# Performance work log

Hardware: AMD Instinct MI355X
Metric: run time of the kernel (lower is better)

Reference implementation:

```python
import jax, jax.numpy as jnp
import numpy as np

N_NODES = 50000
N_EDGES = 800000
D_IN, D_HID, N_CLS = 128, 64, 40


def setup_inputs() -> dict:
    key = jax.random.key(0)
    ks = jax.random.split(key, 12)
    x = jax.random.normal(ks[0], (N_NODES, D_IN), dtype=jnp.float32)
    edge_index = jax.random.randint(ks[1], (2, N_EDGES), 0, N_NODES, dtype=jnp.int64)
    s = 0.05
    return {
        "x": x,
        "edge_index": edge_index,
        # layer 1 params
        "W1": jax.random.normal(ks[2], (D_IN, D_HID), dtype=jnp.float32) * s,
        "aW1": jax.random.normal(ks[3], (2 * D_HID, 1), dtype=jnp.float32) * s,
        "ab1": jnp.zeros((1,), dtype=jnp.float32),
        "b1": jnp.zeros((D_HID,), dtype=jnp.float32),
        # layer 2 params
        "W2": jax.random.normal(ks[4], (D_HID, D_HID), dtype=jnp.float32) * s,
        "aW2": jax.random.normal(ks[5], (2 * D_HID, 1), dtype=jnp.float32) * s,
        "ab2": jnp.zeros((1,), dtype=jnp.float32),
        "b2": jnp.zeros((D_HID,), dtype=jnp.float32),
        # output head
        "Wo": jax.random.normal(ks[6], (D_HID, N_CLS), dtype=jnp.float32) * s,
        "bo": jnp.zeros((N_CLS,), dtype=jnp.float32),
    }


def _gat_layer(x, src, dst, W, aW, ab, bias, n_nodes):
    h = x @ W                                    # [N, out]
    s = h[src]                                   # [E, out] gather source feats
    t = h[dst]                                   # [E, out] gather target feats
    # per-edge attention score, leaky_relu(negative_slope=0.2)
    sim = jax.nn.leaky_relu(jnp.concatenate([s, t], axis=-1) @ aW + ab,
                            negative_slope=0.2)[:, 0]        # [E]
    # scatter-softmax over incoming edges of each dst node
    m = jax.ops.segment_max(sim, dst, num_segments=n_nodes)   # [N]
    e = jnp.exp(sim - m[dst])
    z = jax.ops.segment_sum(e, dst, num_segments=n_nodes)     # [N]
    a = e / z[dst]                                             # [E]
    msg = a[:, None] * s                                       # [E, out]
    out = jax.ops.segment_max(msg, dst, num_segments=n_nodes)  # scatter-max aggr
    return out + bias


def reference(x, edge_index, W1, aW1, ab1, b1, W2, aW2, ab2, b2, Wo, bo):
    n = x.shape[0]
    loop = jnp.arange(n, dtype=edge_index.dtype)
    src = jnp.concatenate([edge_index[0], loop])  # add self loops
    dst = jnp.concatenate([edge_index[1], loop])
    h = jax.nn.relu(_gat_layer(x, src, dst, W1, aW1, ab1, b1, n))
    h = jax.nn.relu(_gat_layer(h, src, dst, W2, aW2, ab2, b2, n))
    logits = h @ Wo + bo
    return jax.nn.log_softmax(logits, axis=-1)
```

## Files before the change

kernel.cpp:

```cpp
#include <hip/hip_runtime.h>
#include <hip/hip_fp16.h>
#include <math.h>

#define N_NODES 50000
#define N_EDGES 800000
#define E_TOT   (N_EDGES + N_NODES)
#define D_HID   64
#define N_CLS   40
#define SCAN_B  256
#define N_CHUNKS ((N_NODES + SCAN_B - 1) / SCAN_B)
#define NB      391
#define EPB     4096

struct __align__(8) H4 { __half2 a, b; };

__device__ __forceinline__ unsigned pk_max_f16(unsigned a, unsigned b) {
    unsigned r;
    asm("v_pk_max_f16 %0, %1, %2" : "=v"(r) : "v"(a), "v"(b));
    return r;
}
__device__ __forceinline__ unsigned pk_mul_f16(unsigned a, unsigned b) {
    unsigned r;
    asm("v_pk_mul_f16 %0, %1, %2" : "=v"(r) : "v"(a), "v"(b));
    return r;
}
__device__ __forceinline__ unsigned pkmax_xor(unsigned v, int o) {
    unsigned t = __shfl_xor((int)v, o, 64);
    return pk_max_f16(v, t);
}

__global__ void k_convert(const void* ei, int2* __restrict__ pairs,
                          int* __restrict__ deg) {
    __shared__ int s_is32;
    if (threadIdx.x == 0) s_is32 = 0;
    __syncthreads();
    const int* p32 = (const int*)ei;
    if (p32[2 * threadIdx.x + 1] != 0) atomicOr(&s_is32, 1);
    __syncthreads();
    int e = blockIdx.x * 256 + threadIdx.x;
    if (e >= N_EDGES) return;
    int s, d;
    if (s_is32) {
        s = p32[e]; d = p32[N_EDGES + e];
    } else {
        const long long* p64 = (const long long*)ei;
        s = (int)p64[e]; d = (int)p64[N_EDGES + e];
    }
    pairs[e] = make_int2(s, d);
    atomicAdd(&deg[d], 1);
}

__device__ __forceinline__ int block_scan_incl(int v, int* wsum) {
    int lane = threadIdx.x & 63, w = threadIdx.x >> 6;
    int s = v;
#pragma unroll
    for (int d = 1; d < 64; d <<= 1) {
        int t = __shfl_up(s, d, 64);
        if (lane >= d) s += t;
    }
    if (lane == 63) wsum[w] = s;
    __syncthreads();
    int add = 0;
    for (int ww = 0; ww < (threadIdx.x >> 6); ++ww) add += wsum[ww];
    return s + add;
}

__global__ void k_scan1(const int* __restrict__ deg, int* __restrict__ rowptr,
                        int* __restrict__ partials) {
    __shared__ int wsum[4];
    int i = blockIdx.x * SCAN_B + threadIdx.x;
    int v = (i < N_NODES) ? deg[i] + 1 : 0;
    int s = block_scan_incl(v, wsum);
    if (i < N_NODES) rowptr[i] = s - v;
    if (threadIdx.x == SCAN_B - 1) partials[blockIdx.x] = s;
}

__global__ void k_scan2(int* partials) {
    __shared__ int wsum[4];
    int i = threadIdx.x;
    int v = (i < N_CHUNKS) ? partials[i] : 0;
    int s = block_scan_incl(v, wsum);
    if (i < N_CHUNKS) partials[i] = s - v;
}

__global__ void k_scan3(const int* __restrict__ partials, int* __restrict__ rowptr) {
    int i = blockIdx.x * SCAN_B + threadIdx.x;
    if (i < N_NODES) rowptr[i] += partials[blockIdx.x];
    if (blockIdx.x == 0 && threadIdx.x == 0) rowptr[N_NODES] = E_TOT;
}

__global__ void k_bucket_init(const int* __restrict__ rowptr, int* __restrict__ bcursor) {
    int b = threadIdx.x;
    if (b < NB) bcursor[b] = rowptr[b << 7] - (b << 7);
}

__global__ __launch_bounds__(256) void k_bucket_scatter(
        const int2* __restrict__ pairs_in, int* __restrict__ bcursor,
        int2* __restrict__ pairs_bkt) {
    __shared__ int counts[512];
    __shared__ int gbase[512];
    int t = threadIdx.x;
    counts[t] = 0; counts[t + 256] = 0;
    __syncthreads();
    int base = blockIdx.x * EPB;
    int nEdge = min(EPB, N_EDGES - base);
    int2 pr0, pr1, pr2, pr3, pr4, pr5, pr6, pr7, pr8, pr9, prA, prB, prC, prD, prE, prF;
    int rk[16], bk[16];
#define LOADI(i, pv) { int idx = t + (i) * 256;                        \
        if (idx < nEdge) { pv = pairs_in[base + idx];                   \
            bk[i] = pv.y >> 7; rk[i] = atomicAdd(&counts[bk[i]], 1); } }
    LOADI(0, pr0) LOADI(1, pr1) LOADI(2, pr2) LOADI(3, pr3)
    LOADI(4, pr4) LOADI(5, pr5) LOADI(6, pr6) LOADI(7, pr7)
    LOADI(8, pr8) LOADI(9, pr9) LOADI(10, prA) LOADI(11, prB)
    LOADI(12, prC) LOADI(13, prD) LOADI(14, prE) LOADI(15, prF)
#undef LOADI
    __syncthreads();
    if (counts[t])       gbase[t]       = atomicAdd(&bcursor[t], counts[t]);
    if (counts[t + 256]) gbase[t + 256] = atomicAdd(&bcursor[t + 256], counts[t + 256]);
    __syncthreads();
#define STOREI(i, pv) { int idx = t + (i) * 256;                        \
        if (idx < nEdge) pairs_bkt[gbase[bk[i]] + rk[i]] = pv; }
    STOREI(0, pr0) STOREI(1, pr1) STOREI(2, pr2) STOREI(3, pr3)
    STOREI(4, pr4) STOREI(5, pr5) STOREI(6, pr6) STOREI(7, pr7)
    STOREI(8, pr8) STOREI(9, pr9) STOREI(10, prA) STOREI(11, prB)
    STOREI(12, prC) STOREI(13, prD) STOREI(14, prE) STOREI(15, prF)
#undef STOREI
}

__global__ __launch_bounds__(256) void k_bucket_place(
        const int2* __restrict__ pairs_bkt, const int* __restrict__ rowptr,
        int* __restrict__ src_sorted) {
    __shared__ int cur[128];
    int b = blockIdx.x, t = threadIdx.x;
    int d0 = b << 7;
    int dEnd = min(d0 + 128, N_NODES);
    if (t < 128) {
        int d = d0 + t;
        if (d < dEnd) {
            int r = rowptr[d];
            src_sorted[r] = d;
            cur[t] = r + 1;
        }
    }
    __syncthreads();
    int pbase = rowptr[d0] - d0;
    int pend  = rowptr[dEnd] - dEnd;
    for (int idx = pbase + t; idx < pend; idx += 256) {
        int2 p = pairs_bkt[idx];
        int pos = atomicAdd(&cur[p.y - d0], 1);
        src_sorted[pos] = p.x;
    }
}

template<int K>
__global__ __launch_bounds__(256, 4) void k_gemm_alpha(
        const float* __restrict__ x, const float* __restrict__ W,
        const float* __restrict__ aW,
        H4* __restrict__ WhH,
        float* __restrict__ alpha_s, float* __restrict__ alpha_t) {
    __shared__ float Wc[32][68];
    __shared__ float xT[32][68];
    int tid = threadIdx.x;
    int tx2 = tid & 15, ty2 = tid >> 4;
    int rowBase = blockIdx.x * 64;

    float acc[4][4];
#pragma unroll
    for (int r = 0; r < 4; ++r)
#pragma unroll
        for (int c = 0; c < 4; ++c) acc[r][c] = 0.f;

    int rr = tid >> 2;
    int kk = (tid & 3) * 8;
    int srcRow = min(rowBase + rr, N_NODES - 1);
    const float* xrow = x + (size_t)srcRow * K;
    int wrow = tid >> 3;
    int wcol = (tid & 7) * 8;

    for (int kb = 0; kb < K; kb += 32) {
        __syncthreads();
        float4 a0 = *(const float4*)(xrow + kb + kk);
        float4 a1 = *(const float4*)(xrow + kb + kk + 4);
        float4 w0 = *(const float4*)(W + (size_t)(kb + wrow) * 64 + wcol);
        float4 w1 = *(const float4*)(W + (size_t)(kb + wrow) * 64 + wcol + 4);
        xT[kk + 0][rr] = a0.x; xT[kk + 1][rr] = a0.y;
        xT[kk + 2][rr] = a0.z; xT[kk + 3][rr] = a0.w;
        xT[kk + 4][rr] = a1.x; xT[kk + 5][rr] = a1.y;
        xT[kk + 6][rr] = a1.z; xT[kk + 7][rr] = a1.w;
        *(float4*)&Wc[wrow][wcol] = w0;
        *(float4*)&Wc[wrow][wcol + 4] = w1;
        __syncthreads();
#pragma unroll 8
        for (int k2 = 0; k2 < 32; ++k2) {
            float4 xa = *(const float4*)&xT[k2][ty2 * 4];
            float4 wb = *(const float4*)&Wc[k2][tx2 * 4];
            acc[0][0] = fmaf(xa.x, wb.x, acc[0][0]);
            acc[0][1] = fmaf(xa.x, wb.y, acc[0][1]);
            acc[0][2] = fmaf(xa.x, wb.z, acc[0][2]);
            acc[0][3] = fmaf(xa.x, wb.w, acc[0][3]);
            acc[1][0] = fmaf(xa.y, wb.x, acc[1][0]);
            acc[1][1] = fmaf(xa.y, wb.y, acc[1][1]);
            acc[1][2] = fmaf(xa.y, wb.z, acc[1][2]);
            acc[1][3] = fmaf(xa.y, wb.w, acc[1][3]);
            acc[2][0] = fmaf(xa.z, wb.x, acc[2][0]);
            acc[2][1] = fmaf(xa.z, wb.y, acc[2][1]);
            acc[2][2] = fmaf(xa.z, wb.z, acc[2][2]);
            acc[2][3] = fmaf(xa.z, wb.w, acc[2][3]);
            acc[3][0] = fmaf(xa.w, wb.x, acc[3][0]);
            acc[3][1] = fmaf(xa.w, wb.y, acc[3][1]);
            acc[3][2] = fmaf(xa.w, wb.z, acc[3][2]);
            acc[3][3] = fmaf(xa.w, wb.w, acc[3][3]);
        }
    }

    float4 as4 = *(const float4*)(aW + tx2 * 4);
    float4 at4 = *(const float4*)(aW + 64 + tx2 * 4);
#pragma unroll
    for (int r = 0; r < 4; ++r) {
        int row = rowBase + ty2 * 4 + r;
        if (row >= N_NODES) continue;
        H4 hv;
        hv.a = __floats2half2_rn(acc[r][0], acc[r][1]);
        hv.b = __floats2half2_rn(acc[r][2], acc[r][3]);
        WhH[(size_t)row * 16 + tx2] = hv;
        float ps = acc[r][0] * as4.x + acc[r][1] * as4.y + acc[r][2] * as4.z + acc[r][3] * as4.w;
        float pt = acc[r][0] * at4.x + acc[r][1] * at4.y + acc[r][2] * at4.z + acc[r][3] * at4.w;
#pragma unroll
        for (int o = 1; o < 16; o <<= 1) {
            ps += __shfl_xor(ps, o, 64);
            pt += __shfl_xor(pt, o, 64);
        }
        if (tx2 == 0) { alpha_s[row] = ps; alpha_t[row] = pt; }
    }
}

__device__ void slow_node(int rs, int re, const int* __restrict__ src_sorted,
                          const float* __restrict__ alpha_s, float at,
                          const H4* __restrict__ WhH, int lane, int fl2,
                          float& z, unsigned vm[4]) {
    float m = -INFINITY;
    for (int base = rs; base < re; base += 64) {
        int idx = base + lane;
        float sim = -INFINITY;
        if (idx < re) {
            int sv = src_sorted[idx];
            float t = alpha_s[sv] + at;
            sim = t > 0.f ? t : 0.2f * t;
        }
#pragma unroll
        for (int o = 32; o; o >>= 1) sim = fmaxf(sim, __shfl_xor(sim, o, 64));
        m = fmaxf(m, sim);
    }
    z = 0.f;
    float vsc = -INFINITY;
    for (int base = rs; base < re; base += 64) {
        int idx = base + lane;
        int cnt = min(64, re - base);
        int svv = 0;
        float ev = 0.f;
        if (idx < re) {
            svv = src_sorted[idx];
            float t = alpha_s[svv] + at;
            t = t > 0.f ? t : 0.2f * t;
            ev = __expf(t - m);
        }
        float sz = ev;
#pragma unroll
        for (int o = 32; o; o >>= 1) sz += __shfl_xor(sz, o, 64);
        z += sz;
        for (int j = 0; j < cnt; ++j) {
            int sj = __shfl(svv, j, 64);
            float ej = __shfl(ev, j, 64);
            float v = __half2float(((const __half*)WhH)[(size_t)sj * 64 + lane]);
            vsc = fmaxf(vsc, ej * v);
        }
    }
#pragma unroll
    for (int q = 0; q < 4; ++q) {
        float a0 = __shfl(vsc, fl2 * 8 + 2 * q, 64);
        float a1 = __shfl(vsc, fl2 * 8 + 2 * q + 1, 64);
        __half2 p = __floats2half2_rn(a0, a1);
        vm[q] = *(unsigned*)&p;
    }
}

template<int HEAD>
__global__ void k_node_aggr(const int* __restrict__ rowptr, const int* __restrict__ src_sorted,
                            const float* __restrict__ alpha_s, const float* __restrict__ alpha_t,
                            const float* __restrict__ ab, const H4* __restrict__ WhH,
                            const float* __restrict__ bias,
                            const float* __restrict__ Wo, const float* __restrict__ bo,
                            float* __restrict__ outp) {
    __shared__ float sWo[HEAD ? 64 * N_CLS : 1];
    __shared__ float sh[HEAD ? 8 * 64 : 1];
    int lane = threadIdx.x, w = threadIdx.y;
    if (HEAD) {
        int tid = w * 64 + lane;
        for (int i = tid; i < 64 * N_CLS; i += 256) sWo[i] = Wo[i];
    }
    int dA = blockIdx.x * 8 + w * 2;
    int dB = dA + 1;
    int rsA = rowptr[dA], reA = rowptr[dA + 1];
    int rsB = rowptr[dB], reB = rowptr[dB + 1];
    int degA = reA - rsA, degB = reB - rsB;
    float abv = ab[0];
    float atA = alpha_t[dA] + abv;
    float atB = alpha_t[dB] + abv;
    int g2 = lane >> 3, fl2 = lane & 7;
    const char* whb = (const char*)WhH;

    float zA, zB;
    unsigned vmA[4], vmB[4];

    if (degA <= 64 && degB <= 64) {
        int svA = src_sorted[rsA + min(lane, degA - 1)];
        int svB = src_sorted[rsB + min(lane, degB - 1)];
        float tA = alpha_s[svA] + atA; tA = tA > 0.f ? tA : 0.2f * tA;
        float tB = alpha_s[svB] + atB; tB = tB > 0.f ? tB : 0.2f * tB;
        float evA = __expf(tA);
        float evB = __expf(tB);
        float zzA = (lane < degA) ? evA : 0.f;
        float zzB = (lane < degB) ? evB : 0.f;
#pragma unroll
        for (int o = 32; o; o >>= 1) {
            zzA += __shfl_xor(zzA, o, 64);
            zzB += __shfl_xor(zzB, o, 64);
        }
        zA = zzA; zB = zzB;
        int ofsA = svA * 128, ofsB = svB * 128;

        const unsigned NEGINF2 = 0xFC00FC00u;
        unsigned vA0 = NEGINF2, vA1 = NEGINF2, vA2 = NEGINF2, vA3 = NEGINF2;
        unsigned vB0 = NEGINF2, vB1 = NEGINF2, vB2 = NEGINF2, vB3 = NEGINF2;
#define ROUND(ev, ofs, deg, v0, v1, v2, v3, r) { \
        int j = (r) * 8 + g2; j = j < (deg) ? j : (deg) - 1;              \
        float ej = __shfl((ev), j, 64);                                   \
        int ro = __shfl((ofs), j, 64);                                    \
        uint4 hv = *(const uint4*)(whb + ro + fl2 * 16);                  \
        __half2 ejh = __float2half2_rn(ej);                               \
        unsigned ej2 = *(unsigned*)&ejh;                                  \
        v0 = pk_max_f16(v0, pk_mul_f16(ej2, hv.x));                       \
        v1 = pk_max_f16(v1, pk_mul_f16(ej2, hv.y));                       \
        v2 = pk_max_f16(v2, pk_mul_f16(ej2, hv.z));                       \
        v3 = pk_max_f16(v3, pk_mul_f16(ej2, hv.w)); }
#define RA(r) ROUND(evA, ofsA, degA, vA0, vA1, vA2, vA3, r)
#define RB(r) ROUND(evB, ofsB, degB, vB0, vB1, vB2, vB3, r)

        RA(0) RB(0) RA(1) RB(1)
        if (degA > 16) { RA(2) RA(3) }
        if (degB > 16) { RB(2) RB(3) }
        if (degA > 32) { RA(4) RA(5) RA(6) RA(7) }
        if (degB > 32) { RB(4) RB(5) RB(6) RB(7) }
#undef RA
#undef RB
#undef ROUND
#pragma unroll
        for (int o = 8; o <= 32; o <<= 1) {
            vA0 = pkmax_xor(vA0, o); vA1 = pkmax_xor(vA1, o);
            vA2 = pkmax_xor(vA2, o); vA3 = pkmax_xor(vA3, o);
            vB0 = pkmax_xor(vB0, o); vB1 = pkmax_xor(vB1, o);
            vB2 = pkmax_xor(vB2, o); vB3 = pkmax_xor(vB3, o);
        }
        vmA[0] = vA0; vmA[1] = vA1; vmA[2] = vA2; vmA[3] = vA3;
        vmB[0] = vB0; vmB[1] = vB1; vmB[2] = vB2; vmB[3] = vB3;
    } else {
        slow_node(rsA, reA, src_sorted, alpha_s, atA, WhH, lane, fl2, zA, vmA);
        slow_node(rsB, reB, src_sorted, alpha_s, atB, WhH, lane, fl2, zB, vmB);
    }

    float4 b0 = *(const float4*)(bias + fl2 * 8);
    float4 b1 = *(const float4*)(bias + fl2 * 8 + 4);
    float rzA = 1.0f / zA, rzB = 1.0f / zB;
    float h8A[8], h8B[8];
#pragma unroll
    for (int q = 0; q < 4; ++q) {
        float2 fa = __half22float2(*(__half2*)&vmA[q]);
        float2 fb = __half22float2(*(__half2*)&vmB[q]);
        h8A[2 * q] = fa.x; h8A[2 * q + 1] = fa.y;
        h8B[2 * q] = fb.x; h8B[2 * q + 1] = fb.y;
    }
    float bias8[8] = { b0.x, b0.y, b0.z, b0.w, b1.x, b1.y, b1.z, b1.w };
#pragma unroll
    for (int q = 0; q < 8; ++q) {
        h8A[q] = fmaxf(h8A[q] * rzA + bias8[q], 0.f);
        h8B[q] = fmaxf(h8B[q] * rzB + bias8[q], 0.f);
    }

    if (!HEAD) {
        if (g2 == 0) {
            float* op = outp + (size_t)dA * 64 + fl2 * 8;
            *(float4*)op = make_float4(h8A[0], h8A[1], h8A[2], h8A[3]);
            *(float4*)(op + 4) = make_float4(h8A[4], h8A[5], h8A[6], h8A[7]);
        } else if (g2 == 1) {
            float* op = outp + (size_t)dB * 64 + fl2 * 8;
            *(float4*)op = make_float4(h8B[0], h8B[1], h8B[2], h8B[3]);
            *(float4*)(op + 4) = make_float4(h8B[4], h8B[5], h8B[6], h8B[7]);
        }
    } else {
        if (g2 == 0) {
            float* sp = sh + (2 * w) * 64 + fl2 * 8;
            *(float4*)sp = make_float4(h8A[0], h8A[1], h8A[2], h8A[3]);
            *(float4*)(sp + 4) = make_float4(h8A[4], h8A[5], h8A[6], h8A[7]);
        } else if (g2 == 1) {
            float* sp = sh + (2 * w + 1) * 64 + fl2 * 8;
            *(float4*)sp = make_float4(h8B[0], h8B[1], h8B[2], h8B[3]);
            *(float4*)(sp + 4) = make_float4(h8B[4], h8B[5], h8B[6], h8B[7]);
        }
        __syncthreads();
#pragma unroll
        for (int n = 0; n < 2; ++n) {
            int dd = dA + n;
            const float* hrow = sh + (2 * w + n) * 64;
            float logit = -INFINITY;
            if (lane < N_CLS) {
                float acc = bo[lane];
#pragma unroll
                for (int k = 0; k < 64; ++k)
                    acc = fmaf(hrow[k], sWo[k * N_CLS + lane], acc);
                logit = acc;
            }
            float mx = logit;
#pragma unroll
            for (int o = 32; o; o >>= 1) mx = fmaxf(mx, __shfl_xor(mx, o, 64));
            float ex = (lane < N_CLS) ? __expf(logit - mx) : 0.f;
            float sm = ex;
#pragma unroll
            for (int o = 32; o; o >>= 1) sm += __shfl_xor(sm, o, 64);
            float lse = mx + __logf(sm);
            if (lane < N_CLS) outp[(size_t)dd * N_CLS + lane] = logit - lse;
        }
    }
}

extern "C" void kernel_launch(void* const* d_in, const int* in_sizes, int n_in,
                              void* d_out, int out_size, void* d_ws, size_t ws_size,
                              hipStream_t stream) {
    const float* x   = (const float*)d_in[0];
    const void*  ei  = d_in[1];
    const float* W1  = (const float*)d_in[2];
    const float* aW1 = (const float*)d_in[3];
    const float* ab1 = (const float*)d_in[4];
    const float* b1  = (const float*)d_in[5];
    const float* W2  = (const float*)d_in[6];
    const float* aW2 = (const float*)d_in[7];
    const float* ab2 = (const float*)d_in[8];
    const float* b2  = (const float*)d_in[9];
    const float* Wo  = (const float*)d_in[10];
    const float* bo  = (const float*)d_in[11];
    float* out = (float*)d_out;

    char* ws = (char*)d_ws;
    size_t off = 0;
    auto alloc = [&](size_t bytes) {
        void* p = ws + off;
        off += (bytes + 255) & ~(size_t)255;
        return p;
    };
    int2*  pairs      = (int2*)alloc((size_t)N_EDGES * 8);
    int2*  pairs_bkt  = (int2*)alloc((size_t)N_EDGES * 8);
    int*   deg        = (int*)alloc((size_t)N_NODES * 4);
    int*   rowptr     = (int*)alloc((size_t)(N_NODES + 1) * 4);
    int*   bcursor    = (int*)alloc((size_t)512 * 4);
    int*   partials   = (int*)alloc((size_t)SCAN_B * 4);
    int*   src_sorted = (int*)alloc((size_t)E_TOT * 4);
    H4*    WhH        = (H4*)alloc((size_t)N_NODES * 64 * 2);
    float* h_mid      = (float*)alloc((size_t)N_NODES * 64 * 4);
    float* alpha_s    = (float*)alloc((size_t)N_NODES * 4);
    float* alpha_t    = (float*)alloc((size_t)N_NODES * 4);

    const int B = 256;
    int gEdgeE = (N_EDGES + B - 1) / B;
    int gPassC = (N_EDGES + EPB - 1) / EPB;
    dim3 blk2(64, 4);
    int gRow  = N_NODES / 8;
    int gGemm = (N_NODES + 63) / 64;

    hipMemsetAsync(deg, 0, (size_t)N_NODES * 4, stream);
    k_convert<<<gEdgeE, B, 0, stream>>>(ei, pairs, deg);
    k_scan1<<<N_CHUNKS, SCAN_B, 0, stream>>>(deg, rowptr, partials);
    k_scan2<<<1, SCAN_B, 0, stream>>>(partials);
    k_scan3<<<N_CHUNKS, SCAN_B, 0, stream>>>(partials, rowptr);
    k_bucket_init<<<1, 512, 0, stream>>>(rowptr, bcursor);
    k_bucket_scatter<<<gPassC, B, 0, stream>>>(pairs, bcursor, pairs_bkt);
    k_bucket_place<<<NB, B, 0, stream>>>(pairs_bkt, rowptr, src_sorted);

    k_gemm_alpha<128><<<gGemm, 256, 0, stream>>>(x, W1, aW1, WhH, alpha_s, alpha_t);
    k_node_aggr<0><<<gRow, blk2, 0, stream>>>(rowptr, src_sorted, alpha_s, alpha_t,
                                              ab1, WhH, b1, nullptr, nullptr, h_mid);

    k_gemm_alpha<64><<<gGemm, 256, 0, stream>>>(h_mid, W2, aW2, WhH, alpha_s, alpha_t);
    k_node_aggr<1><<<gRow, blk2, 0, stream>>>(rowptr, src_sorted, alpha_s, alpha_t,
                                              ab2, WhH, b2, Wo, bo, out);
}
```

Baseline: 173.3 us.

## Use bf16 MFMA for node feature GEMM and attention projections

Replaces the scalar-FMA register-tiled fp32 GEMM with a single-shot bf16 MFMA (16x16x32) version. The whole x tile and a transposed W are staged into shared memory as bf16, and each wave computes a 16x64 output slice. The alpha dot products and the fp16 WhH stores are remapped to the MFMA output layout. This lowers the precision of the inputs to bf16 and writes WhH as scattered 2-byte stores, which may lose coalescing.

```diff
diff --git a/kernel.cpp b/kernel.cpp
--- a/kernel.cpp
+++ b/kernel.cpp
@@ -14,6 +14,9 @@
 
 struct __align__(8) H4 { __half2 a, b; };
 
+typedef short bf16x8 __attribute__((ext_vector_type(8)));
+typedef float f32x4  __attribute__((ext_vector_type(4)));
+
 __device__ __forceinline__ unsigned pk_max_f16(unsigned a, unsigned b) {
     unsigned r;
     asm("v_pk_max_f16 %0, %1, %2" : "=v"(r) : "v"(a), "v"(b));
@@ -27,6 +30,15 @@
 __device__ __forceinline__ unsigned pkmax_xor(unsigned v, int o) {
     unsigned t = __shfl_xor((int)v, o, 64);
     return pk_max_f16(v, t);
+}
+
+__device__ __forceinline__ unsigned short f2bf(float f) {
+    unsigned u = __float_as_uint(f);
+    u += 0x7FFFu + ((u >> 16) & 1);
+    return (unsigned short)(u >> 16);
+}
+__device__ __forceinline__ unsigned pk_bf(float a, float b) {
+    return (unsigned)f2bf(a) | ((unsigned)f2bf(b) << 16);
 }
 
 __global__ void k_convert(const void* ei, int2* __restrict__ pairs,
@@ -153,84 +165,80 @@
 }
 
 template<int K>
-__global__ __launch_bounds__(256, 4) void k_gemm_alpha(
+__global__ __launch_bounds__(256) void k_gemm_alpha(
         const float* __restrict__ x, const float* __restrict__ W,
         const float* __restrict__ aW,
         H4* __restrict__ WhH,
         float* __restrict__ alpha_s, float* __restrict__ alpha_t) {
-    __shared__ float Wc[32][68];
-    __shared__ float xT[32][68];
+    __shared__ unsigned short xb[64][K + 8];
+    __shared__ unsigned short wt[64][K + 8];
     int tid = threadIdx.x;
-    int tx2 = tid & 15, ty2 = tid >> 4;
     int rowBase = blockIdx.x * 64;
 
-    float acc[4][4];
-#pragma unroll
-    for (int r = 0; r < 4; ++r)
-#pragma unroll
-        for (int c = 0; c < 4; ++c) acc[r][c] = 0.f;
-
-    int rr = tid >> 2;
-    int kk = (tid & 3) * 8;
-    int srcRow = min(rowBase + rr, N_NODES - 1);
-    const float* xrow = x + (size_t)srcRow * K;
-    int wrow = tid >> 3;
-    int wcol = (tid & 7) * 8;
-
-    for (int kb = 0; kb < K; kb += 32) {
-        __syncthreads();
-        float4 a0 = *(const float4*)(xrow + kb + kk);
-        float4 a1 = *(const float4*)(xrow + kb + kk + 4);
-        float4 w0 = *(const float4*)(W + (size_t)(kb + wrow) * 64 + wcol);
-        float4 w1 = *(const float4*)(W + (size_t)(kb + wrow) * 64 + wcol + 4);
-        xT[kk + 0][rr] = a0.x; xT[kk + 1][rr] = a0.y;
-        xT[kk + 2][rr] = a0.z; xT[kk + 3][rr] = a0.w;
-        xT[kk + 4][rr] = a1.x; xT[kk + 5][rr] = a1.y;
-        xT[kk + 6][rr] = a1.z; xT[kk + 7][rr] = a1.w;
-        *(float4*)&Wc[wrow][wcol] = w0;
-        *(float4*)&Wc[wrow][wcol + 4] = w1;
-        __syncthreads();
-#pragma unroll 8
-        for (int k2 = 0; k2 < 32; ++k2) {
-            float4 xa = *(const float4*)&xT[k2][ty2 * 4];
-            float4 wb = *(const float4*)&Wc[k2][tx2 * 4];
-            acc[0][0] = fmaf(xa.x, wb.x, acc[0][0]);
-            acc[0][1] = fmaf(xa.x, wb.y, acc[0][1]);
-            acc[0][2] = fmaf(xa.x, wb.z, acc[0][2]);
-            acc[0][3] = fmaf(xa.x, wb.w, acc[0][3]);
-            acc[1][0] = fmaf(xa.y, wb.x, acc[1][0]);
-            acc[1][1] = fmaf(xa.y, wb.y, acc[1][1]);
-            acc[1][2] = fmaf(xa.y, wb.z, acc[1][2]);
-            acc[1][3] = fmaf(xa.y, wb.w, acc[1][3]);
-            acc[2][0] = fmaf(xa.z, wb.x, acc[2][0]);
-            acc[2][1] = fmaf(xa.z, wb.y, acc[2][1]);
-            acc[2][2] = fmaf(xa.z, wb.z, acc[2][2]);
-            acc[2][3] = fmaf(xa.z, wb.w, acc[2][3]);
-            acc[3][0] = fmaf(xa.w, wb.x, acc[3][0]);
-            acc[3][1] = fmaf(xa.w, wb.y, acc[3][1]);
-            acc[3][2] = fmaf(xa.w, wb.z, acc[3][2]);
-            acc[3][3] = fmaf(xa.w, wb.w, acc[3][3]);
-        }
-    }
-
-    float4 as4 = *(const float4*)(aW + tx2 * 4);
-    float4 at4 = *(const float4*)(aW + 64 + tx2 * 4);
+    {
+        int rr = tid >> 2;
+        int kc = (tid & 3) * (K / 4);
+        const float* xr = x + (size_t)min(rowBase + rr, N_NODES - 1) * K + kc;
+        unsigned* dst = (unsigned*)&xb[rr][kc];
+#pragma unroll
+        for (int j = 0; j < K / 4; j += 8) {
+            float4 v0 = *(const float4*)(xr + j);
+            float4 v1 = *(const float4*)(xr + j + 4);
+            dst[j / 2 + 0] = pk_bf(v0.x, v0.y);
+            dst[j / 2 + 1] = pk_bf(v0.z, v0.w);
+            dst[j / 2 + 2] = pk_bf(v1.x, v1.y);
+            dst[j / 2 + 3] = pk_bf(v1.z, v1.w);
+        }
+    }
+    for (int i = tid; i < K * 64; i += 256) {
+        int k = i >> 6, n = i & 63;
+        wt[n][k] = f2bf(W[i]);
+    }
+    __syncthreads();
+
+    int w = tid >> 6, lane = tid & 63;
+    int la = lane & 15, hi = lane >> 4;
+
+    f32x4 acc[4];
+#pragma unroll
+    for (int c = 0; c < 4; ++c) acc[c] = (f32x4){0.f, 0.f, 0.f, 0.f};
+
+#pragma unroll
+    for (int t = 0; t < K / 32; ++t) {
+        int k0 = t * 32 + hi * 8;
+        bf16x8 af = *(const bf16x8*)&xb[w * 16 + la][k0];
+#pragma unroll
+        for (int c = 0; c < 4; ++c) {
+            bf16x8 bfr = *(const bf16x8*)&wt[c * 16 + la][k0];
+            acc[c] = __builtin_amdgcn_mfma_f32_16x16x32_bf16(af, bfr, acc[c], 0, 0, 0);
+        }
+    }
+
+    float as4[4], at4[4];
+#pragma unroll
+    for (int c = 0; c < 4; ++c) {
+        as4[c] = aW[c * 16 + la];
+        at4[c] = aW[64 + c * 16 + la];
+    }
 #pragma unroll
     for (int r = 0; r < 4; ++r) {
-        int row = rowBase + ty2 * 4 + r;
-        if (row >= N_NODES) continue;
-        H4 hv;
-        hv.a = __floats2half2_rn(acc[r][0], acc[r][1]);
-        hv.b = __floats2half2_rn(acc[r][2], acc[r][3]);
-        WhH[(size_t)row * 16 + tx2] = hv;
-        float ps = acc[r][0] * as4.x + acc[r][1] * as4.y + acc[r][2] * as4.z + acc[r][3] * as4.w;
-        float pt = acc[r][0] * at4.x + acc[r][1] * at4.y + acc[r][2] * at4.z + acc[r][3] * at4.w;
+        int row = rowBase + w * 16 + hi * 4 + r;
+        float ps = acc[0][r] * as4[0] + acc[1][r] * as4[1]
+                 + acc[2][r] * as4[2] + acc[3][r] * as4[3];
+        float pt = acc[0][r] * at4[0] + acc[1][r] * at4[1]
+                 + acc[2][r] * at4[2] + acc[3][r] * at4[3];
 #pragma unroll
         for (int o = 1; o < 16; o <<= 1) {
             ps += __shfl_xor(ps, o, 64);
             pt += __shfl_xor(pt, o, 64);
         }
-        if (tx2 == 0) { alpha_s[row] = ps; alpha_t[row] = pt; }
+        if (row < N_NODES) {
+            __half* wr = (__half*)&WhH[(size_t)row * 16];
+#pragma unroll
+            for (int c = 0; c < 4; ++c)
+                wr[c * 16 + la] = __float2half(acc[c][r]);
+            if (la == 0) { alpha_s[row] = ps; alpha_t[row] = pt; }
+        }
     }
 }
 
```

Result: faster. 162.9 us (-6.0%).
